# Kernel optimization log

Measured on AMD Instinct MI355X. Metric: run time of the kernel, lower is better.

Reference implementation:

```python
import jax, jax.numpy as jnp
import numpy as np

B, N, NVT, HS, NZ = 512, 256, 32, 128, 64


def setup_inputs() -> dict:
    key = jax.random.key(0)
    ks = jax.random.split(key, 16)
    node_types = jax.random.randint(ks[0], (B, N), 0, NVT, dtype=jnp.int32)
    node_types = node_types.at[:, 0].set(0)      # START_TYPE
    node_types = node_types.at[:, -1].set(1)     # END_TYPE
    adj = jax.random.randint(ks[1], (B, N, N), 0, 2, dtype=jnp.int32)
    # DAG: edges only u -> v with u < v (strict upper triangular)
    tri = jnp.triu(jnp.ones((N, N), jnp.int32), k=1)
    adj = adj * tri[None, :, :]
    s = 0.05
    p = lambda k, shp: (jax.random.normal(k, shp, jnp.float32) * s)
    return {
        "node_types": node_types,
        "adj": adj,
        "W_ih": p(ks[2], (3 * HS, NVT)),   # grue_forward weight_ih
        "W_hh": p(ks[3], (3 * HS, HS)),    # grue_forward weight_hh
        "b_ih": p(ks[4], (3 * HS,)),
        "b_hh": p(ks[5], (3 * HS,)),
        "Wg": p(ks[6], (HS, NVT)),         # gate_forward linear
        "bg": p(ks[7], (HS,)),
        "Wm": p(ks[8], (HS, NVT)),         # mapper_forward (no bias)
        "W1": p(ks[9], (NZ, HS)),          # fc1 -> mu
        "b1": p(ks[10], (NZ,)),
        "W2": p(ks[11], (NZ, HS)),         # fc2 -> logvar
        "b2": p(ks[12], (NZ,)),
    }


def reference(node_types, adj, W_ih, W_hh, b_ih, b_hh, Wg, bg, Wm, W1, b1, W2, b2):
    hs = Wg.shape[0]
    # one-hot vertex types  [B, N, nvt]
    X = jax.nn.one_hot(node_types, Wg.shape[1], dtype=W_ih.dtype)
    # gated message from each vertex's TYPE (mapper has no bias -> padding contributes 0)
    gated = jax.nn.sigmoid(jnp.einsum('bnv,hv->bnh', X, Wg) + bg) \
            * jnp.einsum('bnv,hv->bnh', X, Wm)                      # [B, N, hs]
    A = adj.astype(gated.dtype)
    # predecessor aggregation: H_v = sum_{u: u->v} gated_u
    Hpre = jnp.einsum('buv,buh->bvh', A, gated)                     # [B, N, hs]
    # torch GRUCell(X_v, Hpre_v), vectorized over all vertices (no recurrence:
    # messages depend only on predecessor types)
    gi = jnp.einsum('bnv,gv->bng', X, W_ih) + b_ih                  # [B, N, 3hs]
    gh = jnp.einsum('bnh,gh->bng', Hpre, W_hh) + b_hh
    r = jax.nn.sigmoid(gi[..., :hs] + gh[..., :hs])
    z = jax.nn.sigmoid(gi[..., hs:2 * hs] + gh[..., hs:2 * hs])
    n = jnp.tanh(gi[..., 2 * hs:] + r * gh[..., 2 * hs:])
    Hv = (1.0 - z) * n + z * Hpre                                   # H_forward, [B, N, hs]
    # graph state: sum over vertices [1, N-1) (start=1, end_offset=1)
    Hg = Hv[:, 1:-1, :].sum(axis=1)                                 # [B, hs]
    mu = Hg @ W1.T + b1
    logvar = Hg @ W2.T + b2
    return (mu, logvar)
```

## Files before the change

kernel.cpp:

```cpp
#include <hip/hip_runtime.h>
#include <hip/hip_bf16.h>

#define HS 128
#define NVT 32
#define NN 256

typedef __attribute__((ext_vector_type(8))) short bf16x8;
typedef __attribute__((ext_vector_type(4))) float f32x4;

#define TABB_OFF 0
#define GIT_OFF  32768
#define CNT8_OFF 65536

static __device__ __forceinline__ short f2bs(float f) {
    __hip_bfloat16 h = __float2bfloat16(f);
    short s; __builtin_memcpy(&s, &h, 2);
    return s;
}
static __device__ __forceinline__ float bs2f(short s) {
    __hip_bfloat16 h; __builtin_memcpy(&h, &s, 2);
    return __bfloat162float(h);
}
static __device__ __forceinline__ float sigm(float x) {
    return __builtin_amdgcn_rcpf(1.f + __expf(-x));
}

__global__ void __launch_bounds__(512) build_tables(
    const float* __restrict__ W_ih, const float* __restrict__ W_hh,
    const float* __restrict__ b_ih, const float* __restrict__ b_hh,
    const float* __restrict__ Wg,   const float* __restrict__ bg,
    const float* __restrict__ Wm,
    short* __restrict__ TABB, short* __restrict__ GIT)
{
    __shared__ float G_s[HS];
    const int t = blockIdx.x;
    const int j = threadIdx.x;
    if (j < HS) {
        float x = Wg[j * NVT + t] + bg[j];
        G_s[j] = sigm(x) * Wm[j * NVT + t];
    }
    __syncthreads();
    if (j < 384) {
        float acc = 0.f;
        for (int h = 0; h < HS; ++h) acc += G_s[h] * W_hh[j * HS + h];
        TABB[j * NVT + t] = f2bs(acc);
        float git = W_ih[j * NVT + t] + b_ih[j];
        if (j < 256) git += b_hh[j];
        GIT[t * 384 + j] = f2bs(git);
    } else {
        TABB[j * NVT + t] = f2bs(G_s[j - 384]);
    }
}

__global__ void __launch_bounds__(256) hist_part(
    const int* __restrict__ node_types, const int* __restrict__ adj,
    unsigned char* __restrict__ cnt8)
{
    __shared__ unsigned tmask[NVT * 2];
    const int blk = blockIdx.x;
    const int b = blk >> 2, c = blk & 3;
    const int tid = threadIdx.x;
    const int* adjb = adj + (size_t)b * NN * NN + c * 64 * NN;

    unsigned cb0 = 0, cb1 = 0;
    {
        int av[32];
        #pragma unroll
        for (int j = 0; j < 32; ++j) av[j] = adjb[j * NN + tid];
        #pragma unroll
        for (int j = 0; j < 32; ++j) cb0 |= ((unsigned)av[j]) << j;
        #pragma unroll
        for (int j = 0; j < 32; ++j) av[j] = adjb[(32 + j) * NN + tid];
        #pragma unroll
        for (int j = 0; j < 32; ++j) cb1 |= ((unsigned)av[j]) << j;
    }
    if (tid < 64) {
        int t = tid >> 1, w2 = tid & 1;
        const int* ty = node_types + b * NN + c * 64 + w2 * 32;
        unsigned mw = 0;
        #pragma unroll
        for (int k = 0; k < 32; ++k)
            mw |= ((unsigned)(ty[k] == t)) << k;
        tmask[tid] = mw;
    }
    __syncthreads();

    unsigned outw[8];
    #pragma unroll
    for (int q = 0; q < 8; ++q) {
        unsigned w = 0;
        #pragma unroll
        for (int s = 0; s < 4; ++s) {
            int t = q * 4 + s;
            unsigned cnt = __popc(cb0 & tmask[2 * t]) + __popc(cb1 & tmask[2 * t + 1]);
            w |= cnt << (8 * s);
        }
        outw[q] = w;
    }
    uint4* dst = (uint4*)(cnt8 + ((size_t)blk * NN + tid) * 32);
    dst[0] = make_uint4(outw[0], outw[1], outw[2], outw[3]);
    dst[1] = make_uint4(outw[4], outw[5], outw[6], outw[7]);
}

__global__ void __launch_bounds__(256) dvae_main(
    const int* __restrict__ node_types, const unsigned char* __restrict__ cnt8,
    const short* __restrict__ TABB, const short* __restrict__ GIT,
    const float* __restrict__ b_hh,
    const float* __restrict__ W1, const float* __restrict__ b1,
    const float* __restrict__ W2, const float* __restrict__ b2,
    float* __restrict__ out)
{
    __shared__ unsigned cntA[NN * 20];
    __shared__ short GITs[NVT * 388];
    __shared__ int types_s[NN];
    __shared__ float hg_s[HS];

    const int b = blockIdx.x, tid = threadIdx.x;
    const int wave = tid >> 6, lane = tid & 63;
    const int quad = lane >> 4, col = lane & 15;

    types_s[tid] = node_types[b * NN + tid];

    {
        uint4 a0, a1;
        {
            const uint4* s = (const uint4*)(cnt8 + ((size_t)(b * 4 + 0) * NN + tid) * 32);
            a0 = s[0]; a1 = s[1];
        }
        #pragma unroll
        for (int c = 1; c < 4; ++c) {
            const uint4* s = (const uint4*)(cnt8 + ((size_t)(b * 4 + c) * NN + tid) * 32);
            uint4 p0 = s[0], p1 = s[1];
            a0.x += p0.x; a0.y += p0.y; a0.z += p0.z; a0.w += p0.w;
            a1.x += p1.x; a1.y += p1.y; a1.z += p1.z; a1.w += p1.w;
        }
        unsigned acc8[8] = {a0.x, a0.y, a0.z, a0.w, a1.x, a1.y, a1.z, a1.w};
        #pragma unroll
        for (int q = 0; q < 8; ++q) {
            unsigned u = acc8[q];
            float f0 = (float)(u & 0xFF),         f1 = (float)((u >> 8) & 0xFF);
            float f2 = (float)((u >> 16) & 0xFF), f3 = (float)((u >> 24) & 0xFF);
            cntA[tid * 20 + 2 * q]     = (__float_as_uint(f0) >> 16) | (__float_as_uint(f1) & 0xFFFF0000u);
            cntA[tid * 20 + 2 * q + 1] = (__float_as_uint(f2) >> 16) | (__float_as_uint(f3) & 0xFFFF0000u);
        }
    }

    {
        const unsigned* src = (const unsigned*)GIT;
        unsigned* dst = (unsigned*)GITs;
        #pragma unroll
        for (int c = 0; c < 24; ++c) {
            int i = c * 256 + tid;
            int t = i / 192, j = i - t * 192;
            dst[t * 194 + j] = src[i];
        }
    }

    bf16x8 bfrag[8];
    #pragma unroll
    for (int i = 0; i < 8; ++i) {
        int gate = i >> 1, sub = (i & 1) * 16;
        int jb = (gate < 3 ? gate * 128 : 384) + wave * 32 + sub;
        bfrag[i] = *(const bf16x8*)(TABB + (jb + col) * 32 + quad * 8);
    }
    const int h0 = wave * 32 + col;
    const float bhn0 = b_hh[256 + h0], bhn1 = b_hh[256 + h0 + 16];
    float hg0 = 0.f, hg1 = 0.f;
    __syncthreads();

    for (int m = 0; m < 16; ++m) {
        bf16x8 afrag = *(const bf16x8*)(cntA + (m * 16 + col) * 20 + quad * 4);
        f32x4 acc[8];
        #pragma unroll
        for (int i = 0; i < 8; ++i)
            acc[i] = __builtin_amdgcn_mfma_f32_16x16x32_bf16(
                afrag, bfrag[i], (f32x4){0.f, 0.f, 0.f, 0.f}, 0, 0, 0);
        #pragma unroll
        for (int r = 0; r < 4; ++r) {
            int vv = m * 16 + quad * 4 + r;
            int tv = types_s[vv];
            float msk = (vv >= 1 && vv < NN - 1) ? 1.f : 0.f;
            const short* g = GITs + tv * 388;
            {
                float rr = sigm(bs2f(g[h0]) + acc[0][r]);
                float zz = sigm(bs2f(g[128 + h0]) + acc[2][r]);
                float x2 = bs2f(g[256 + h0]) + rr * (acc[4][r] + bhn0);
                float nt = 1.f - 2.f * __builtin_amdgcn_rcpf(1.f + __expf(2.f * x2));
                hg0 += msk * ((1.f - zz) * nt + zz * acc[6][r]);
            }
            {
                int h1 = h0 + 16;
                float rr = sigm(bs2f(g[h1]) + acc[1][r]);
                float zz = sigm(bs2f(g[128 + h1]) + acc[3][r]);
                float x2 = bs2f(g[256 + h1]) + rr * (acc[5][r] + bhn1);
                float nt = 1.f - 2.f * __builtin_amdgcn_rcpf(1.f + __expf(2.f * x2));
                hg1 += msk * ((1.f - zz) * nt + zz * acc[7][r]);
            }
        }
    }
    hg0 += __shfl_xor(hg0, 16); hg0 += __shfl_xor(hg0, 32);
    hg1 += __shfl_xor(hg1, 16); hg1 += __shfl_xor(hg1, 32);
    if (lane < 16) { hg_s[h0] = hg0; hg_s[h0 + 16] = hg1; }
    __syncthreads();

    if (tid < 128) {
        int which = tid >> 6, zz = tid & 63;
        const float* W = which ? W2 : W1;
        float acc2 = which ? b2[zz] : b1[zz];
        const float4* Wv = (const float4*)(W + zz * HS);
        #pragma unroll
        for (int i = 0; i < 32; ++i) {
            float4 ww = Wv[i];
            acc2 += hg_s[4 * i] * ww.x + hg_s[4 * i + 1] * ww.y
                  + hg_s[4 * i + 2] * ww.z + hg_s[4 * i + 3] * ww.w;
        }
        out[which * 32768 + b * 64 + zz] = acc2;
    }
}

extern "C" void kernel_launch(void* const* d_in, const int* in_sizes, int n_in,
                              void* d_out, int out_size, void* d_ws, size_t ws_size,
                              hipStream_t stream)
{
    const int* node_types = (const int*)d_in[0];
    const int* adj        = (const int*)d_in[1];
    const float* W_ih = (const float*)d_in[2];
    const float* W_hh = (const float*)d_in[3];
    const float* b_ih = (const float*)d_in[4];
    const float* b_hh = (const float*)d_in[5];
    const float* Wg   = (const float*)d_in[6];
    const float* bg   = (const float*)d_in[7];
    const float* Wm   = (const float*)d_in[8];
    const float* W1   = (const float*)d_in[9];
    const float* b1   = (const float*)d_in[10];
    const float* W2   = (const float*)d_in[11];
    const float* b2   = (const float*)d_in[12];

    char* ws = (char*)d_ws;
    short* TABB = (short*)(ws + TABB_OFF);
    short* GIT  = (short*)(ws + GIT_OFF);
    unsigned char* cnt8 = (unsigned char*)(ws + CNT8_OFF);
    float* out  = (float*)d_out;

    build_tables<<<dim3(32), dim3(512), 0, stream>>>(W_ih, W_hh, b_ih, b_hh, Wg, bg, Wm, TABB, GIT);
    hist_part<<<dim3(2048), dim3(256), 0, stream>>>(node_types, adj, cnt8);
    dvae_main<<<dim3(512), dim3(256), 0, stream>>>(node_types, cnt8, TABB, GIT, b_hh, W1, b1, W2, b2, out);
}
```

Baseline: 254.4 us.

## Fuse adjacency histogram into main kernel and interleave GRU gate table

Merges the separate histogram kernel into the main per-graph kernel. Each block now reads its graph's full adjacency with 16-byte loads, builds bitmasks, popcounts against per-type masks, and reduces the partial counts through shared memory. This removes the global cnt8 round-trip and one kernel launch. The input-gate table is also reordered so that the three gate values for a (type, h) pair sit together and load as one 8-byte read. In exchange, only 512 blocks now stream the 128MB adjacency, which cuts memory parallelism compared with the 2048-block histogram, and shared memory use rises, which can lower occupancy.

```diff
diff --git a/kernel.cpp b/kernel.cpp
--- a/kernel.cpp
+++ b/kernel.cpp
@@ -6,11 +6,11 @@
 #define NN 256
 
 typedef __attribute__((ext_vector_type(8))) short bf16x8;
+typedef __attribute__((ext_vector_type(4))) short s16x4;
 typedef __attribute__((ext_vector_type(4))) float f32x4;
 
 #define TABB_OFF 0
-#define GIT_OFF  32768
-#define CNT8_OFF 65536
+#define GIT2_OFF 32768
 
 static __device__ __forceinline__ short f2bs(float f) {
     __hip_bfloat16 h = __float2bfloat16(f);
@@ -30,7 +30,7 @@
     const float* __restrict__ b_ih, const float* __restrict__ b_hh,
     const float* __restrict__ Wg,   const float* __restrict__ bg,
     const float* __restrict__ Wm,
-    short* __restrict__ TABB, short* __restrict__ GIT)
+    short* __restrict__ TABB, short* __restrict__ GIT2)
 {
     __shared__ float G_s[HS];
     const int t = blockIdx.x;
@@ -45,73 +45,27 @@
         for (int h = 0; h < HS; ++h) acc += G_s[h] * W_hh[j * HS + h];
         TABB[j * NVT + t] = f2bs(acc);
         float git = W_ih[j * NVT + t] + b_ih[j];
-        if (j < 256) git += b_hh[j];
-        GIT[t * 384 + j] = f2bs(git);
+        int gate = j >> 7, h = j & 127;
+        if (gate < 2) git += b_hh[j];
+        GIT2[(t * 128 + h) * 4 + gate] = f2bs(git);
     } else {
         TABB[j * NVT + t] = f2bs(G_s[j - 384]);
-    }
-}
-
-__global__ void __launch_bounds__(256) hist_part(
+        GIT2[(t * 128 + (j - 384)) * 4 + 3] = 0;
+    }
+}
+
+__global__ void __launch_bounds__(256) dvae_fused(
     const int* __restrict__ node_types, const int* __restrict__ adj,
-    unsigned char* __restrict__ cnt8)
-{
-    __shared__ unsigned tmask[NVT * 2];
-    const int blk = blockIdx.x;
-    const int b = blk >> 2, c = blk & 3;
-    const int tid = threadIdx.x;
-    const int* adjb = adj + (size_t)b * NN * NN + c * 64 * NN;
-
-    unsigned cb0 = 0, cb1 = 0;
-    {
-        int av[32];
-        #pragma unroll
-        for (int j = 0; j < 32; ++j) av[j] = adjb[j * NN + tid];
-        #pragma unroll
-        for (int j = 0; j < 32; ++j) cb0 |= ((unsigned)av[j]) << j;
-        #pragma unroll
-        for (int j = 0; j < 32; ++j) av[j] = adjb[(32 + j) * NN + tid];
-        #pragma unroll
-        for (int j = 0; j < 32; ++j) cb1 |= ((unsigned)av[j]) << j;
-    }
-    if (tid < 64) {
-        int t = tid >> 1, w2 = tid & 1;
-        const int* ty = node_types + b * NN + c * 64 + w2 * 32;
-        unsigned mw = 0;
-        #pragma unroll
-        for (int k = 0; k < 32; ++k)
-            mw |= ((unsigned)(ty[k] == t)) << k;
-        tmask[tid] = mw;
-    }
-    __syncthreads();
-
-    unsigned outw[8];
-    #pragma unroll
-    for (int q = 0; q < 8; ++q) {
-        unsigned w = 0;
-        #pragma unroll
-        for (int s = 0; s < 4; ++s) {
-            int t = q * 4 + s;
-            unsigned cnt = __popc(cb0 & tmask[2 * t]) + __popc(cb1 & tmask[2 * t + 1]);
-            w |= cnt << (8 * s);
-        }
-        outw[q] = w;
-    }
-    uint4* dst = (uint4*)(cnt8 + ((size_t)blk * NN + tid) * 32);
-    dst[0] = make_uint4(outw[0], outw[1], outw[2], outw[3]);
-    dst[1] = make_uint4(outw[4], outw[5], outw[6], outw[7]);
-}
-
-__global__ void __launch_bounds__(256) dvae_main(
-    const int* __restrict__ node_types, const unsigned char* __restrict__ cnt8,
-    const short* __restrict__ TABB, const short* __restrict__ GIT,
+    const short* __restrict__ TABB, const short* __restrict__ GIT2,
     const float* __restrict__ b_hh,
     const float* __restrict__ W1, const float* __restrict__ b1,
     const float* __restrict__ W2, const float* __restrict__ b2,
     float* __restrict__ out)
 {
     __shared__ unsigned cntA[NN * 20];
-    __shared__ short GITs[NVT * 388];
+    __shared__ short GITs[NVT * 512];
+    __shared__ unsigned pc[4 * NN * 8];
+    __shared__ unsigned tmask[NVT * 8];
     __shared__ int types_s[NN];
     __shared__ float hg_s[HS];
 
@@ -122,52 +76,95 @@
     types_s[tid] = node_types[b * NN + tid];
 
     {
-        uint4 a0, a1;
-        {
-            const uint4* s = (const uint4*)(cnt8 + ((size_t)(b * 4 + 0) * NN + tid) * 32);
-            a0 = s[0]; a1 = s[1];
-        }
-        #pragma unroll
-        for (int c = 1; c < 4; ++c) {
-            const uint4* s = (const uint4*)(cnt8 + ((size_t)(b * 4 + c) * NN + tid) * 32);
-            uint4 p0 = s[0], p1 = s[1];
-            a0.x += p0.x; a0.y += p0.y; a0.z += p0.z; a0.w += p0.w;
-            a1.x += p1.x; a1.y += p1.y; a1.z += p1.z; a1.w += p1.w;
-        }
-        unsigned acc8[8] = {a0.x, a0.y, a0.z, a0.w, a1.x, a1.y, a1.z, a1.w};
+        const uint4* src = (const uint4*)GIT2;
+        uint4* dst = (uint4*)GITs;
+        #pragma unroll
+        for (int i = 0; i < 8; ++i) dst[i * 256 + tid] = src[i * 256 + tid];
+    }
+    bf16x8 bfrag[8];
+    #pragma unroll
+    for (int i = 0; i < 8; ++i) {
+        int gate = i >> 1, sub = (i & 1) * 16;
+        int jb = (gate < 3 ? gate * 128 : 384) + wave * 32 + sub;
+        bfrag[i] = *(const bf16x8*)(TABB + (jb + col) * 32 + quad * 8);
+    }
+    const int h0 = wave * 32 + col;
+    const float bhn0 = b_hh[256 + h0], bhn1 = b_hh[256 + h0 + 16];
+    __syncthreads();
+
+    {
+        int t = tid >> 3, w8 = tid & 7;
+        const int* ty = types_s + w8 * 32;
+        unsigned mw = 0;
+        #pragma unroll
+        for (int k = 0; k < 32; ++k) mw |= ((unsigned)(ty[k] == t)) << k;
+        tmask[tid] = mw;
+    }
+
+    const uint4* adjb = (const uint4*)(adj + (size_t)b * NN * NN) + wave * 64 * 64 + lane;
+    unsigned cb0a = 0, cb0b = 0, cb1a = 0, cb1b = 0, cb2a = 0, cb2b = 0, cb3a = 0, cb3b = 0;
+    #pragma unroll
+    for (int half = 0; half < 2; ++half) {
+        #pragma unroll
+        for (int bb = 0; bb < 4; ++bb) {
+            uint4 av[8];
+            #pragma unroll
+            for (int j = 0; j < 8; ++j) av[j] = adjb[(half * 32 + bb * 8 + j) * 64];
+            #pragma unroll
+            for (int j = 0; j < 8; ++j) {
+                int sh = bb * 8 + j;
+                if (half == 0) {
+                    cb0a |= av[j].x << sh; cb1a |= av[j].y << sh;
+                    cb2a |= av[j].z << sh; cb3a |= av[j].w << sh;
+                } else {
+                    cb0b |= av[j].x << sh; cb1b |= av[j].y << sh;
+                    cb2b |= av[j].z << sh; cb3b |= av[j].w << sh;
+                }
+            }
+        }
+    }
+    __syncthreads();
+
+    unsigned pcnt[4][8];
+    #pragma unroll
+    for (int k = 0; k < 4; ++k)
+        #pragma unroll
+        for (int q = 0; q < 8; ++q) pcnt[k][q] = 0;
+    #pragma unroll
+    for (int t = 0; t < 32; ++t) {
+        unsigned tm0 = tmask[t * 8 + wave * 2];
+        unsigned tm1 = tmask[t * 8 + wave * 2 + 1];
+        unsigned sh = (unsigned)((t & 3) * 8);
+        pcnt[0][t >> 2] += (__popc(cb0a & tm0) + __popc(cb0b & tm1)) << sh;
+        pcnt[1][t >> 2] += (__popc(cb1a & tm0) + __popc(cb1b & tm1)) << sh;
+        pcnt[2][t >> 2] += (__popc(cb2a & tm0) + __popc(cb2b & tm1)) << sh;
+        pcnt[3][t >> 2] += (__popc(cb3a & tm0) + __popc(cb3b & tm1)) << sh;
+    }
+    {
+        uint4* p4 = (uint4*)pc;
+        #pragma unroll
+        for (int k = 0; k < 4; ++k) {
+            int c = lane * 4 + k;
+            p4[(wave * NN + c) * 2]     = make_uint4(pcnt[k][0], pcnt[k][1], pcnt[k][2], pcnt[k][3]);
+            p4[(wave * NN + c) * 2 + 1] = make_uint4(pcnt[k][4], pcnt[k][5], pcnt[k][6], pcnt[k][7]);
+        }
+    }
+    __syncthreads();
+
+    {
         #pragma unroll
         for (int q = 0; q < 8; ++q) {
-            unsigned u = acc8[q];
+            unsigned u = pc[(0 * NN + tid) * 8 + q] + pc[(1 * NN + tid) * 8 + q]
+                       + pc[(2 * NN + tid) * 8 + q] + pc[(3 * NN + tid) * 8 + q];
             float f0 = (float)(u & 0xFF),         f1 = (float)((u >> 8) & 0xFF);
             float f2 = (float)((u >> 16) & 0xFF), f3 = (float)((u >> 24) & 0xFF);
             cntA[tid * 20 + 2 * q]     = (__float_as_uint(f0) >> 16) | (__float_as_uint(f1) & 0xFFFF0000u);
             cntA[tid * 20 + 2 * q + 1] = (__float_as_uint(f2) >> 16) | (__float_as_uint(f3) & 0xFFFF0000u);
         }
     }
-
-    {
-        const unsigned* src = (const unsigned*)GIT;
-        unsigned* dst = (unsigned*)GITs;
-        #pragma unroll
-        for (int c = 0; c < 24; ++c) {
-            int i = c * 256 + tid;
-            int t = i / 192, j = i - t * 192;
-            dst[t * 194 + j] = src[i];
-        }
-    }
-
-    bf16x8 bfrag[8];
-    #pragma unroll
-    for (int i = 0; i < 8; ++i) {
-        int gate = i >> 1, sub = (i & 1) * 16;
-        int jb = (gate < 3 ? gate * 128 : 384) + wave * 32 + sub;
-        bfrag[i] = *(const bf16x8*)(TABB + (jb + col) * 32 + quad * 8);
-    }
-    const int h0 = wave * 32 + col;
-    const float bhn0 = b_hh[256 + h0], bhn1 = b_hh[256 + h0 + 16];
+    __syncthreads();
+
     float hg0 = 0.f, hg1 = 0.f;
-    __syncthreads();
-
     for (int m = 0; m < 16; ++m) {
         bf16x8 afrag = *(const bf16x8*)(cntA + (m * 16 + col) * 20 + quad * 4);
         f32x4 acc[8];
@@ -180,19 +177,19 @@
             int vv = m * 16 + quad * 4 + r;
             int tv = types_s[vv];
             float msk = (vv >= 1 && vv < NN - 1) ? 1.f : 0.f;
-            const short* g = GITs + tv * 388;
             {
-                float rr = sigm(bs2f(g[h0]) + acc[0][r]);
-                float zz = sigm(bs2f(g[128 + h0]) + acc[2][r]);
-                float x2 = bs2f(g[256 + h0]) + rr * (acc[4][r] + bhn0);
+                s16x4 gg = *(const s16x4*)(GITs + (tv * 128 + h0) * 4);
+                float rr = sigm(bs2f(gg[0]) + acc[0][r]);
+                float zz = sigm(bs2f(gg[1]) + acc[2][r]);
+                float x2 = bs2f(gg[2]) + rr * (acc[4][r] + bhn0);
                 float nt = 1.f - 2.f * __builtin_amdgcn_rcpf(1.f + __expf(2.f * x2));
                 hg0 += msk * ((1.f - zz) * nt + zz * acc[6][r]);
             }
             {
-                int h1 = h0 + 16;
-                float rr = sigm(bs2f(g[h1]) + acc[1][r]);
-                float zz = sigm(bs2f(g[128 + h1]) + acc[3][r]);
-                float x2 = bs2f(g[256 + h1]) + rr * (acc[5][r] + bhn1);
+                s16x4 gg = *(const s16x4*)(GITs + (tv * 128 + h0 + 16) * 4);
+                float rr = sigm(bs2f(gg[0]) + acc[1][r]);
+                float zz = sigm(bs2f(gg[1]) + acc[3][r]);
+                float x2 = bs2f(gg[2]) + rr * (acc[5][r] + bhn1);
                 float nt = 1.f - 2.f * __builtin_amdgcn_rcpf(1.f + __expf(2.f * x2));
                 hg1 += msk * ((1.f - zz) * nt + zz * acc[7][r]);
             }
@@ -238,11 +235,9 @@
 
     char* ws = (char*)d_ws;
     short* TABB = (short*)(ws + TABB_OFF);
-    short* GIT  = (short*)(ws + GIT_OFF);
-    unsigned char* cnt8 = (unsigned char*)(ws + CNT8_OFF);
+    short* GIT2 = (short*)(ws + GIT2_OFF);
     float* out  = (float*)d_out;
 
-    build_tables<<<dim3(32), dim3(512), 0, stream>>>(W_ih, W_hh, b_ih, b_hh, Wg, bg, Wm, TABB, GIT);
-    hist_part<<<dim3(2048), dim3(256), 0, stream>>>(node_types, adj, cnt8);
-    dvae_main<<<dim3(512), dim3(256), 0, stream>>>(node_types, cnt8, TABB, GIT, b_hh, W1, b1, W2, b2, out);
-}
+    build_tables<<<dim3(32), dim3(512), 0, stream>>>(W_ih, W_hh, b_ih, b_hh, Wg, bg, Wm, TABB, GIT2);
+    dvae_fused<<<dim3(512), dim3(256), 0, stream>>>(node_types, adj, TABB, GIT2, b_hh, W1, b1, W2, b2, out);
+}
```

New measurement: 251.2 us. Within noise of the previous version (-1.3%).
